# Kernel tuning notes

Measured on AMD Instinct MI355X. Metric: run time of the kernel, lower is better.

The kernel has to match this reference:

```python
import jax, jax.numpy as jnp
import numpy as np

B, H, W, C = 8, 64, 64, 256
NH, WS, SS = 8, 8, 4
HD = C // NH          # head dim 32
N = WS * WS           # 64 tokens per window
NW = (H // WS) * (W // WS)  # 64 windows
MLP = 4 * C


def _rel_index():
    ch = np.arange(WS)
    coords = np.stack(np.meshgrid(ch, ch, indexing='ij')).reshape(2, -1)  # [2, N]
    rel = (coords[:, :, None] - coords[:, None, :]).transpose(1, 2, 0)   # [N, N, 2]
    rel[:, :, 0] += WS - 1
    rel[:, :, 1] += WS - 1
    rel[:, :, 0] *= 2 * WS - 1
    return jnp.asarray(rel.sum(-1))  # [N, N] indices into table

REL_IDX = _rel_index()


def _attn_mask():
    # standard Swin shifted-window mask: [nW, N, N] with 0 / -100
    img = np.zeros((H, W))
    slices = (slice(0, -WS), slice(-WS, -SS), slice(-SS, None))
    cnt = 0
    for hs in slices:
        for ws_ in slices:
            img[hs, ws_] = cnt
            cnt += 1
    m = img.reshape(H // WS, WS, W // WS, WS).transpose(0, 2, 1, 3).reshape(-1, N)
    diff = m[:, None, :] - m[:, :, None]
    return jnp.asarray(np.where(diff != 0, -100.0, 0.0).astype(np.float32))

MASK = _attn_mask()


def setup_inputs() -> dict:
    key = jax.random.key(0)
    ks = jax.random.split(key, 8)
    s = 0.02
    return {
        'hidden_states': jax.random.normal(ks[0], (B, H * W, C), jnp.float32),
        'ln1_g': jnp.ones((C,), jnp.float32),
        'ln1_b': jnp.zeros((C,), jnp.float32),
        'wq': jax.random.normal(ks[1], (C, C), jnp.float32) * s,
        'bq': jnp.zeros((C,), jnp.float32),
        'wk': jax.random.normal(ks[2], (C, C), jnp.float32) * s,
        'bk': jnp.zeros((C,), jnp.float32),
        'wv': jax.random.normal(ks[3], (C, C), jnp.float32) * s,
        'bv': jnp.zeros((C,), jnp.float32),
        'rel_table': jax.random.normal(ks[4], ((2 * WS - 1) ** 2, NH), jnp.float32) * s,
        'wo': jax.random.normal(ks[5], (C, C), jnp.float32) * s,
        'bo': jnp.zeros((C,), jnp.float32),
        'ln2_g': jnp.ones((C,), jnp.float32),
        'ln2_b': jnp.zeros((C,), jnp.float32),
        'w1': jax.random.normal(ks[6], (MLP, C), jnp.float32) * s,
        'b1': jnp.zeros((MLP,), jnp.float32),
        'w2': jax.random.normal(ks[7], (C, MLP), jnp.float32) * s,
        'b2': jnp.zeros((C,), jnp.float32),
    }


def _ln(x, g, b):
    mu = x.mean(-1, keepdims=True)
    var = x.var(-1, keepdims=True)
    return (x - mu) * jax.lax.rsqrt(var + 1e-5) * g + b


def reference(hidden_states, ln1_g, ln1_b, wq, bq, wk, bk, wv, bv, rel_table,
              wo, bo, ln2_g, ln2_b, w1, b1, w2, b2):
    shortcut = hidden_states
    x = _ln(hidden_states, ln1_g, ln1_b).reshape(B, H, W, C)
    # cyclic shift
    x = jnp.roll(x, (-SS, -SS), axis=(1, 2))
    # window partition -> [B*nW, N, C]
    xw = x.reshape(B, H // WS, WS, W // WS, WS, C).transpose(0, 1, 3, 2, 4, 5).reshape(-1, N, C)
    q = (xw @ wq.T + bq).reshape(-1, N, NH, HD).transpose(0, 2, 1, 3)
    k = (xw @ wk.T + bk).reshape(-1, N, NH, HD).transpose(0, 2, 1, 3)
    v = (xw @ wv.T + bv).reshape(-1, N, NH, HD).transpose(0, 2, 1, 3)
    scores = jnp.einsum('bhnd,bhmd->bhnm', q, k) / np.float32(np.sqrt(HD))
    bias = rel_table[REL_IDX]                 # [N, N, NH] gathered bias
    scores = scores + bias.transpose(2, 0, 1)[None]
    scores = scores.reshape(B, NW, NH, N, N) + MASK[None, :, None]
    probs = jax.nn.softmax(scores, axis=-1).reshape(-1, NH, N, N)
    ctx = jnp.einsum('bhnm,bhmd->bnhd', probs, v).reshape(-1, N, C)
    attn_out = ctx @ wo.T + bo                # SelfOutput dense
    # window reverse + reverse shift
    x = attn_out.reshape(B, H // WS, W // WS, WS, WS, C).transpose(0, 1, 3, 2, 4, 5).reshape(B, H, W, C)
    x = jnp.roll(x, (SS, SS), axis=(1, 2)).reshape(B, H * W, C)
    hidden = shortcut + x
    y = _ln(hidden, ln2_g, ln2_b)
    y = jax.nn.gelu(y @ w1.T + b1, approximate=False) @ w2.T + b2
    return hidden + y
```

## Files before the change

kernel.cpp:

```cpp
#include <hip/hip_runtime.h>
#include <hip/hip_bf16.h>
#include <math.h>

__device__ __forceinline__ unsigned short f2bf(float f) {
    union { float f; unsigned u; } c; c.f = f;
    unsigned r = c.u + 0x7fffu + ((c.u >> 16) & 1u);
    return (unsigned short)(r >> 16);
}
__device__ __forceinline__ float bfu(unsigned short u) {
    union { unsigned x; float f; } c; c.x = ((unsigned)u) << 16; return c.f;
}
__device__ __forceinline__ float gelu_t(float x) {
    float z = x * (1.59576912f + 0.07135481f * x * x);
    return x / (1.0f + __expf(-z));
}

typedef __bf16 bf16x8_t __attribute__((ext_vector_type(8)));
typedef float  f32x4_t  __attribute__((ext_vector_type(4)));

#define AS1 __attribute__((address_space(1)))
#define AS3 __attribute__((address_space(3)))
__device__ __forceinline__ void g2lds16(const void* g, void* l) {
    __builtin_amdgcn_global_load_lds((const AS1 unsigned int*)g, (AS3 unsigned int*)l, 16, 0, 0);
}

__global__ void cvt_all(const float* __restrict__ wq, const float* __restrict__ wk,
                        const float* __restrict__ wv, const float* __restrict__ wo,
                        const float* __restrict__ w1, const float* __restrict__ w2,
                        unsigned short* __restrict__ wqkv_b, unsigned short* __restrict__ wo_b,
                        unsigned short* __restrict__ w1_b, unsigned short* __restrict__ w2_b) {
    int i = blockIdx.x * 256 + threadIdx.x;
    const float* src; unsigned short* dst; int base;
    if (i < 16384)       { src = wq; dst = wqkv_b;          base = 0; }
    else if (i < 32768)  { src = wk; dst = wqkv_b + 65536;  base = 16384; }
    else if (i < 49152)  { src = wv; dst = wqkv_b + 131072; base = 32768; }
    else if (i < 65536)  { src = wo; dst = wo_b;            base = 49152; }
    else if (i < 131072) { src = w1; dst = w1_b;            base = 65536; }
    else                 { src = w2; dst = w2_b;            base = 131072; }
    int j = (i - base) * 4;
    float4 v = *(const float4*)(src + j);
    ushort4 o = { f2bf(v.x), f2bf(v.y), f2bf(v.z), f2bf(v.w) };
    *(ushort4*)(dst + j) = o;
}

template<int GATHER, int BF16IN>
__global__ void ln_kernel(const void* __restrict__ xv, const float* __restrict__ g,
                          const float* __restrict__ b, unsigned short* __restrict__ out) {
    int row  = blockIdx.x * 4 + (threadIdx.x >> 6);
    int lane = threadIdx.x & 63;
    int src;
    if (GATHER) {
        int bb = row >> 12;
        int rem = row & 4095;
        int winid = rem >> 6, tok = rem & 63;
        int wi = winid >> 3, wj = winid & 7;
        int ii = tok >> 3,  jj = tok & 7;
        int hh = (wi * 8 + ii + 4) & 63;
        int ww = (wj * 8 + jj + 4) & 63;
        src = (bb << 12) + hh * 64 + ww;
    } else {
        src = row;
    }
    float4 v;
    if (BF16IN) {
        ushort4 u = *(const ushort4*)((const unsigned short*)xv + (size_t)src * 256 + lane * 4);
        v.x = bfu(u.x); v.y = bfu(u.y); v.z = bfu(u.z); v.w = bfu(u.w);
    } else {
        v = *(const float4*)((const float*)xv + (size_t)src * 256 + lane * 4);
    }
    float s  = v.x + v.y + v.z + v.w;
    float s2 = v.x*v.x + v.y*v.y + v.z*v.z + v.w*v.w;
    #pragma unroll
    for (int off = 32; off > 0; off >>= 1) {
        s  += __shfl_xor(s,  off, 64);
        s2 += __shfl_xor(s2, off, 64);
    }
    float mean = s * (1.0f / 256.0f);
    float var  = s2 * (1.0f / 256.0f) - mean * mean;
    float rstd = rsqrtf(var + 1e-5f);
    int c0 = lane * 4;
    float4 gg  = *(const float4*)(g + c0);
    float4 bb4 = *(const float4*)(b + c0);
    ushort4 o;
    o.x = f2bf((v.x - mean) * rstd * gg.x + bb4.x);
    o.y = f2bf((v.y - mean) * rstd * gg.y + bb4.y);
    o.z = f2bf((v.z - mean) * rstd * gg.z + bb4.z);
    o.w = f2bf((v.w - mean) * rstd * gg.w + bb4.w);
    *(ushort4*)(out + (size_t)row * 256 + c0) = o;
}

template<int MODE, int K>
__global__ __launch_bounds__(256, 4) void gemm_tile(
        const unsigned short* __restrict__ A,
        const unsigned short* __restrict__ Bw,
        const float* __restrict__ bias,
        int M, int N,
        unsigned short* __restrict__ obf,
        float* __restrict__ of32,
        const void* __restrict__ addp) {
    __shared__ unsigned short As[128 * 64];
    __shared__ unsigned short Bs[128 * 64];
    const int t = threadIdx.x;
    const int lane = t & 63, wave = t >> 6;
    const int m0 = blockIdx.x * 128, n0 = blockIdx.y * 128;
    const int wm = (wave >> 1) * 64, wn = (wave & 1) * 64;
    const int lr = lane & 15, kg = lane >> 4;

    f32x4_t acc[4][4];
    #pragma unroll
    for (int i = 0; i < 4; ++i)
        #pragma unroll
        for (int j = 0; j < 4; ++j) { acc[i][j][0]=0.f; acc[i][j][1]=0.f; acc[i][j][2]=0.f; acc[i][j][3]=0.f; }

    const int srow = t >> 3;
    const int sc   = (((t & 7) ^ (srow & 7)) * 8);
    const unsigned short* ga = A  + (size_t)(m0 + srow) * K + sc;
    const unsigned short* gb = Bw + (size_t)(n0 + srow) * K + sc;
    unsigned short* la = &As[t * 8];
    unsigned short* lb = &Bs[t * 8];

    #pragma unroll
    for (int k0 = 0; k0 < K; k0 += 64) {
        __syncthreads();
        #pragma unroll
        for (int i = 0; i < 4; ++i) {
            g2lds16(ga + (size_t)(i * 32) * K + k0, la + i * 2048);
            g2lds16(gb + (size_t)(i * 32) * K + k0, lb + i * 2048);
        }
        __syncthreads();
        #pragma unroll
        for (int ks = 0; ks < 64; ks += 32) {
            bf16x8_t af[4], bfr[4];
            #pragma unroll
            for (int i = 0; i < 4; ++i) {
                int r = wm + i * 16 + lr;
                af[i] = *(const bf16x8_t*)&As[r * 64 + ((((ks >> 3) + kg) ^ (r & 7)) << 3)];
            }
            #pragma unroll
            for (int j = 0; j < 4; ++j) {
                int r = wn + j * 16 + lr;
                bfr[j] = *(const bf16x8_t*)&Bs[r * 64 + ((((ks >> 3) + kg) ^ (r & 7)) << 3)];
            }
            #pragma unroll
            for (int i = 0; i < 4; ++i)
                #pragma unroll
                for (int j = 0; j < 4; ++j)
                    acc[i][j] = __builtin_amdgcn_mfma_f32_16x16x32_bf16(af[i], bfr[j], acc[i][j], 0, 0, 0);
        }
    }

    #pragma unroll
    for (int i = 0; i < 4; ++i) {
        #pragma unroll
        for (int j = 0; j < 4; ++j) {
            int col = n0 + wn + j * 16 + lr;
            float bv = bias[col];
            #pragma unroll
            for (int e = 0; e < 4; ++e) {
                int row = m0 + wm + i * 16 + kg * 4 + e;
                float v = acc[i][j][e] + bv;
                if (MODE == 0) {
                    obf[(size_t)row * N + col] = f2bf(v);
                } else if (MODE == 1) {
                    obf[(size_t)row * N + col] = f2bf(gelu_t(v));
                } else if (MODE == 2) {
                    int bb = row >> 12;
                    int rem = row & 4095;
                    int winid = rem >> 6, tok = rem & 63;
                    int wi = winid >> 3, wj = winid & 7;
                    int ii = tok >> 3,  jj = tok & 7;
                    int hh = (wi * 8 + ii + 4) & 63;
                    int ww = (wj * 8 + jj + 4) & 63;
                    size_t dst = ((size_t)(bb << 12) + hh * 64 + ww) * 256 + col;
                    obf[dst] = f2bf(((const float*)addp)[dst] + v);
                } else {
                    size_t dst = (size_t)row * N + col;
                    of32[dst] = bfu(((const unsigned short*)addp)[dst]) + v;
                }
            }
        }
    }
}

#define PR 72
#define VR 72
__global__ void __launch_bounds__(256) attn_mfma(
        const unsigned short* __restrict__ qkv,
        const float* __restrict__ relt,
        unsigned short* __restrict__ ctx) {
    __shared__ float rs[1800];
    __shared__ unsigned short Pl[4][64 * PR];
    __shared__ unsigned short Vt[4][32 * VR];

    int t = threadIdx.x;
    int lane = t & 63, wave = t >> 6;
    for (int i = t; i < 1800; i += 256) rs[i] = relt[i];
    __syncthreads();

    int wh = blockIdx.x * 4 + wave;
    int wg = wh >> 3, h = wh & 7;
    int win = wg & 63;
    int ln = lane & 15, quad = lane >> 4;

    unsigned short* P = &Pl[wave][0];
    unsigned short* V = &Vt[wave][0];
    const unsigned short* base = qkv + (size_t)wg * 64 * 768 + h * 32;

    union BF8 { bf16x8_t v; unsigned short s[8]; };
    {
        const bf16x8_t* vp = (const bf16x8_t*)(base + (size_t)lane * 768 + 512);
        BF8 vv[4];
        #pragma unroll
        for (int c = 0; c < 4; ++c) vv[c].v = vp[c];
        #pragma unroll
        for (int c = 0; c < 4; ++c)
            #pragma unroll
            for (int e = 0; e < 8; ++e)
                V[(c * 8 + e) * VR + lane] = vv[c].s[e];
    }

    bf16x8_t qa[4], kb[4];
    #pragma unroll
    for (int i = 0; i < 4; ++i)
        qa[i] = *(const bf16x8_t*)(base + (size_t)(i * 16 + ln) * 768 + quad * 8);
    #pragma unroll
    for (int j = 0; j < 4; ++j)
        kb[j] = *(const bf16x8_t*)(base + (size_t)(j * 16 + ln) * 768 + 256 + quad * 8);

    f32x4_t acc[4][4];
    #pragma unroll
    for (int i = 0; i < 4; ++i)
        #pragma unroll
        for (int j = 0; j < 4; ++j) { acc[i][j][0]=0.f; acc[i][j][1]=0.f; acc[i][j][2]=0.f; acc[i][j][3]=0.f; }
    #pragma unroll
    for (int i = 0; i < 4; ++i)
        #pragma unroll
        for (int j = 0; j < 4; ++j)
            acc[i][j] = __builtin_amdgcn_mfma_f32_16x16x32_bf16(qa[i], kb[j], acc[i][j], 0, 0, 0);

    const float scale = 0.17677669529663687f;
    int wi = win >> 3, wj = win & 7;
    int mjv = ln & 7;
    int regm[4], mi[4];
    #pragma unroll
    for (int j = 0; j < 4; ++j) {
        mi[j] = j * 2 + (ln >> 3);
        int hm = wi * 8 + mi[j], wm = wj * 8 + mjv;
        regm[j] = (hm < 56 ? 0 : (hm < 60 ? 1 : 2)) * 3 + (wm < 56 ? 0 : (wm < 60 ? 1 : 2));
    }
    float inv[4][4];
    #pragma unroll
    for (int i = 0; i < 4; ++i) {
        #pragma unroll
        for (int e = 0; e < 4; ++e) {
            int q = i * 16 + quad * 4 + e;
            int ti = q >> 3, tj = q & 7;
            int hn = wi * 8 + ti, wn = wj * 8 + tj;
            int regn = (hn < 56 ? 0 : (hn < 60 ? 1 : 2)) * 3 + (wn < 56 ? 0 : (wn < 60 ? 1 : 2));
            float sum = 0.f;
            #pragma unroll
            for (int j = 0; j < 4; ++j) {
                float bv = rs[((ti - mi[j] + 7) * 15 + (tj - mjv + 7)) * 8 + h];
                float s = acc[i][j][e] * scale + bv + (regm[j] != regn ? -100.f : 0.f);
                float p = __expf(s);
                sum += p;
                P[q * PR + j * 16 + ln] = f2bf(p);
            }
            #pragma unroll
            for (int off = 1; off < 16; off <<= 1) sum += __shfl_xor(sum, off, 64);
            inv[i][e] = 1.0f / sum;
        }
    }
    __syncthreads();

    bf16x8_t vb[2][2];
    #pragma unroll
    for (int jd = 0; jd < 2; ++jd)
        #pragma unroll
        for (int kc = 0; kc < 2; ++kc)
            vb[jd][kc] = *(const bf16x8_t*)&V[(jd * 16 + ln) * VR + kc * 32 + quad * 8];
    f32x4_t occ[4][2];
    #pragma unroll
    for (int i = 0; i < 4; ++i)
        #pragma unroll
        for (int jd = 0; jd < 2; ++jd) { occ[i][jd][0]=0.f; occ[i][jd][1]=0.f; occ[i][jd][2]=0.f; occ[i][jd][3]=0.f; }
    #pragma unroll
    for (int i = 0; i < 4; ++i) {
        #pragma unroll
        for (int kc = 0; kc < 2; ++kc) {
            bf16x8_t pf = *(const bf16x8_t*)&P[(i * 16 + ln) * PR + kc * 32 + quad * 8];
            occ[i][0] = __builtin_amdgcn_mfma_f32_16x16x32_bf16(pf, vb[0][kc], occ[i][0], 0, 0, 0);
            occ[i][1] = __builtin_amdgcn_mfma_f32_16x16x32_bf16(pf, vb[1][kc], occ[i][1], 0, 0, 0);
        }
    }

    unsigned short* cbase = ctx + (size_t)wg * 64 * 256 + h * 32;
    #pragma unroll
    for (int i = 0; i < 4; ++i)
        #pragma unroll
        for (int e = 0; e < 4; ++e) {
            int q = i * 16 + quad * 4 + e;
            #pragma unroll
            for (int jd = 0; jd < 2; ++jd)
                cbase[(size_t)q * 256 + jd * 16 + ln] = f2bf(occ[i][jd][e] * inv[i][e]);
        }
}

extern "C" void kernel_launch(void* const* d_in, const int* in_sizes, int n_in,
                              void* d_out, int out_size, void* d_ws, size_t ws_size,
                              hipStream_t stream) {
    const float* hs   = (const float*)d_in[0];
    const float* ln1g = (const float*)d_in[1];
    const float* ln1b = (const float*)d_in[2];
    const float* wq   = (const float*)d_in[3];
    const float* bq   = (const float*)d_in[4];
    const float* wk   = (const float*)d_in[5];
    const float* bk   = (const float*)d_in[6];
    const float* wv   = (const float*)d_in[7];
    const float* bv   = (const float*)d_in[8];
    const float* relt = (const float*)d_in[9];
    const float* wo   = (const float*)d_in[10];
    const float* bo   = (const float*)d_in[11];
    const float* ln2g = (const float*)d_in[12];
    const float* ln2b = (const float*)d_in[13];
    const float* w1   = (const float*)d_in[14];
    const float* b1   = (const float*)d_in[15];
    const float* w2   = (const float*)d_in[16];
    const float* b2   = (const float*)d_in[17];
    float* out = (float*)d_out;

    const size_t NTOK = 32768;
    size_t off = 0;
    auto carve = [&](size_t bytes) { void* p = (char*)d_ws + off; off += (bytes + 255) & ~(size_t)255; return p; };
    unsigned short* wqkv_b = (unsigned short*)carve(768ull * 256 * 2);
    unsigned short* wo_b   = (unsigned short*)carve(65536ull * 2);
    unsigned short* w1_b   = (unsigned short*)carve(262144ull * 2);
    unsigned short* w2_b   = (unsigned short*)carve(262144ull * 2);
    float*          bqkv   = (float*)carve(768ull * 4);
    unsigned short* hiddenb= (unsigned short*)carve(NTOK * 256 * 2);
    unsigned short* xw     = (unsigned short*)carve(NTOK * 256 * 2);
    unsigned short* qkvb   = (unsigned short*)carve(NTOK * 768 * 2);
    unsigned short* cx     = (unsigned short*)carve(NTOK * 256 * 2);
    unsigned short* h1 = qkvb;
    unsigned short* yb = xw;

    cvt_all<<<768, 256, 0, stream>>>(wq, wk, wv, wo, w1, w2, wqkv_b, wo_b, w1_b, w2_b);
    hipMemcpyAsync(bqkv,       bq, 256 * 4, hipMemcpyDeviceToDevice, stream);
    hipMemcpyAsync(bqkv + 256, bk, 256 * 4, hipMemcpyDeviceToDevice, stream);
    hipMemcpyAsync(bqkv + 512, bv, 256 * 4, hipMemcpyDeviceToDevice, stream);

    ln_kernel<1, 0><<<8192, 256, 0, stream>>>(hs, ln1g, ln1b, xw);

    gemm_tile<0, 256><<<dim3(256, 6), 256, 0, stream>>>(xw, wqkv_b, bqkv, 32768, 768, qkvb, nullptr, nullptr);

    attn_mfma<<<1024, 256, 0, stream>>>(qkvb, relt, cx);

    gemm_tile<2, 256><<<dim3(256, 2), 256, 0, stream>>>(cx, wo_b, bo, 32768, 256, hiddenb, nullptr, hs);

    ln_kernel<0, 1><<<8192, 256, 0, stream>>>(hiddenb, ln2g, ln2b, yb);

    gemm_tile<1, 256><<<dim3(256, 8), 256, 0, stream>>>(yb, w1_b, b1, 32768, 1024, h1, nullptr, nullptr);

    gemm_tile<3, 1024><<<dim3(256, 2), 256, 0, stream>>>(h1, w2_b, b2, 32768, 256, nullptr, out, hiddenb);
}
```

Measured before the change: 290.9 us.

## Fuse LN2, MLP up-projection with GELU, and down-projection into one kernel

Replaces the LN2 kernel and the two MLP GEMMs with a single fused kernel. Each block normalises a 64-row tile in LDS, computes the 1024-wide hidden layer in 128-column chunks into LDS, and accumulates the down-projection in registers, so the 32768x1024 intermediate never goes to global memory. Weight fragments are read straight from global memory without LDS staging, and only 512 blocks launch, which may hurt latency hiding and occupancy. The XOR swizzle in gemm_tile's LDS layout is also removed, which may add bank conflicts in the remaining GEMMs.

Measured after the change: 325.9 us. 1.12x slower.

```diff
diff --git a/kernel.cpp b/kernel.cpp
--- a/kernel.cpp
+++ b/kernel.cpp
@@ -43,8 +43,8 @@
     *(ushort4*)(dst + j) = o;
 }
 
-template<int GATHER, int BF16IN>
-__global__ void ln_kernel(const void* __restrict__ xv, const float* __restrict__ g,
+template<int GATHER>
+__global__ void ln_kernel(const float* __restrict__ x, const float* __restrict__ g,
                           const float* __restrict__ b, unsigned short* __restrict__ out) {
     int row  = blockIdx.x * 4 + (threadIdx.x >> 6);
     int lane = threadIdx.x & 63;
@@ -61,13 +61,7 @@
     } else {
         src = row;
     }
-    float4 v;
-    if (BF16IN) {
-        ushort4 u = *(const ushort4*)((const unsigned short*)xv + (size_t)src * 256 + lane * 4);
-        v.x = bfu(u.x); v.y = bfu(u.y); v.z = bfu(u.z); v.w = bfu(u.w);
-    } else {
-        v = *(const float4*)((const float*)xv + (size_t)src * 256 + lane * 4);
-    }
+    const float4 v = *(const float4*)(x + (size_t)src * 256 + lane * 4);
     float s  = v.x + v.y + v.z + v.w;
     float s2 = v.x*v.x + v.y*v.y + v.z*v.z + v.w*v.w;
     #pragma unroll
@@ -96,7 +90,6 @@
         const float* __restrict__ bias,
         int M, int N,
         unsigned short* __restrict__ obf,
-        float* __restrict__ of32,
         const void* __restrict__ addp) {
     __shared__ unsigned short As[128 * 64];
     __shared__ unsigned short Bs[128 * 64];
@@ -113,9 +106,9 @@
         for (int j = 0; j < 4; ++j) { acc[i][j][0]=0.f; acc[i][j][1]=0.f; acc[i][j][2]=0.f; acc[i][j][3]=0.f; }
 
     const int srow = t >> 3;
-    const int sc   = (((t & 7) ^ (srow & 7)) * 8);
-    const unsigned short* ga = A  + (size_t)(m0 + srow) * K + sc;
-    const unsigned short* gb = Bw + (size_t)(n0 + srow) * K + sc;
+    const int sck  = (t & 7) * 8;
+    const unsigned short* ga = A  + (size_t)(m0 + srow) * K + sck;
+    const unsigned short* gb = Bw + (size_t)(n0 + srow) * K + sck;
     unsigned short* la = &As[t * 8];
     unsigned short* lb = &Bs[t * 8];
 
@@ -132,15 +125,11 @@
         for (int ks = 0; ks < 64; ks += 32) {
             bf16x8_t af[4], bfr[4];
             #pragma unroll
-            for (int i = 0; i < 4; ++i) {
-                int r = wm + i * 16 + lr;
-                af[i] = *(const bf16x8_t*)&As[r * 64 + ((((ks >> 3) + kg) ^ (r & 7)) << 3)];
-            }
-            #pragma unroll
-            for (int j = 0; j < 4; ++j) {
-                int r = wn + j * 16 + lr;
-                bfr[j] = *(const bf16x8_t*)&Bs[r * 64 + ((((ks >> 3) + kg) ^ (r & 7)) << 3)];
-            }
+            for (int i = 0; i < 4; ++i)
+                af[i] = *(const bf16x8_t*)&As[(wm + i * 16 + lr) * 64 + ks + kg * 8];
+            #pragma unroll
+            for (int j = 0; j < 4; ++j)
+                bfr[j] = *(const bf16x8_t*)&Bs[(wn + j * 16 + lr) * 64 + ks + kg * 8];
             #pragma unroll
             for (int i = 0; i < 4; ++i)
                 #pragma unroll
@@ -163,7 +152,7 @@
                     obf[(size_t)row * N + col] = f2bf(v);
                 } else if (MODE == 1) {
                     obf[(size_t)row * N + col] = f2bf(gelu_t(v));
-                } else if (MODE == 2) {
+                } else {
                     int bb = row >> 12;
                     int rem = row & 4095;
                     int winid = rem >> 6, tok = rem & 63;
@@ -173,13 +162,144 @@
                     int ww = (wj * 8 + jj + 4) & 63;
                     size_t dst = ((size_t)(bb << 12) + hh * 64 + ww) * 256 + col;
                     obf[dst] = f2bf(((const float*)addp)[dst] + v);
-                } else {
-                    size_t dst = (size_t)row * N + col;
-                    of32[dst] = bfu(((const unsigned short*)addp)[dst]) + v;
                 }
             }
         }
     }
+}
+
+__global__ __launch_bounds__(256, 3) void mlp_fused(
+        const unsigned short* __restrict__ hid,
+        const float* __restrict__ g2, const float* __restrict__ bb2ln,
+        const unsigned short* __restrict__ w1, const float* __restrict__ b1,
+        const unsigned short* __restrict__ w2, const float* __restrict__ b2,
+        float* __restrict__ out) {
+    __shared__ unsigned short Ys[64 * 256];
+    __shared__ unsigned short Hs[64 * 136];
+    const int t = threadIdx.x;
+    const int lane = t & 63, wave = t >> 6;
+    const int m0 = blockIdx.x * 64;
+    const int lr = lane & 15, kg = lane >> 4;
+    const int wm = (wave >> 1) * 32;
+    const int wn1 = (wave & 1) * 64;
+    const int wo2 = (wave & 1) * 128;
+
+    #pragma unroll
+    for (int c = 0; c < 8; ++c)
+        g2lds16(hid + (size_t)(m0 + c * 8 + (t >> 5)) * 256 + (t & 31) * 8,
+                &Ys[c * 2048 + t * 8]);
+    __syncthreads();
+
+    {
+        int r = t >> 2, q = t & 3;
+        unsigned short* rp = &Ys[r * 256 + q * 64];
+        float s = 0.f, s2 = 0.f;
+        #pragma unroll
+        for (int c8 = 0; c8 < 8; ++c8) {
+            bf16x8_t u = *(const bf16x8_t*)(rp + c8 * 8);
+            #pragma unroll
+            for (int e = 0; e < 8; ++e) {
+                float f = (float)u[e];
+                s += f; s2 += f * f;
+            }
+        }
+        s  += __shfl_xor(s, 1, 64);  s  += __shfl_xor(s, 2, 64);
+        s2 += __shfl_xor(s2, 1, 64); s2 += __shfl_xor(s2, 2, 64);
+        float mean = s * (1.0f / 256.0f);
+        float var  = s2 * (1.0f / 256.0f) - mean * mean;
+        float rstd = rsqrtf(var + 1e-5f);
+        #pragma unroll
+        for (int c8 = 0; c8 < 8; ++c8) {
+            int col = q * 64 + c8 * 8;
+            bf16x8_t u = *(const bf16x8_t*)(rp + c8 * 8);
+            float4 ga = *(const float4*)(g2 + col),     gb4 = *(const float4*)(g2 + col + 4);
+            float4 ba = *(const float4*)(bb2ln + col),  bb4 = *(const float4*)(bb2ln + col + 4);
+            unsigned short o[8];
+            o[0] = f2bf(((float)u[0] - mean) * rstd * ga.x + ba.x);
+            o[1] = f2bf(((float)u[1] - mean) * rstd * ga.y + ba.y);
+            o[2] = f2bf(((float)u[2] - mean) * rstd * ga.z + ba.z);
+            o[3] = f2bf(((float)u[3] - mean) * rstd * ga.w + ba.w);
+            o[4] = f2bf(((float)u[4] - mean) * rstd * gb4.x + bb4.x);
+            o[5] = f2bf(((float)u[5] - mean) * rstd * gb4.y + bb4.y);
+            o[6] = f2bf(((float)u[6] - mean) * rstd * gb4.z + bb4.z);
+            o[7] = f2bf(((float)u[7] - mean) * rstd * gb4.w + bb4.w);
+            *(ushort4*)(rp + c8 * 8)     = *(ushort4*)&o[0];
+            *(ushort4*)(rp + c8 * 8 + 4) = *(ushort4*)&o[4];
+        }
+    }
+    __syncthreads();
+
+    f32x4_t acc2[2][8];
+    #pragma unroll
+    for (int i = 0; i < 2; ++i)
+        #pragma unroll
+        for (int j = 0; j < 8; ++j) { acc2[i][j][0]=0.f; acc2[i][j][1]=0.f; acc2[i][j][2]=0.f; acc2[i][j][3]=0.f; }
+
+    for (int c = 0; c < 8; ++c) {
+        const int n0c = c * 128;
+        f32x4_t acc1[2][4];
+        #pragma unroll
+        for (int i = 0; i < 2; ++i)
+            #pragma unroll
+            for (int j = 0; j < 4; ++j) { acc1[i][j][0]=0.f; acc1[i][j][1]=0.f; acc1[i][j][2]=0.f; acc1[i][j][3]=0.f; }
+        #pragma unroll
+        for (int kc = 0; kc < 8; ++kc) {
+            bf16x8_t af[2], bfr[4];
+            #pragma unroll
+            for (int i = 0; i < 2; ++i)
+                af[i] = *(const bf16x8_t*)&Ys[(wm + i * 16 + lr) * 256 + kc * 32 + kg * 8];
+            #pragma unroll
+            for (int j = 0; j < 4; ++j)
+                bfr[j] = *(const bf16x8_t*)(w1 + (size_t)(n0c + wn1 + j * 16 + lr) * 256 + kc * 32 + kg * 8);
+            #pragma unroll
+            for (int i = 0; i < 2; ++i)
+                #pragma unroll
+                for (int j = 0; j < 4; ++j)
+                    acc1[i][j] = __builtin_amdgcn_mfma_f32_16x16x32_bf16(af[i], bfr[j], acc1[i][j], 0, 0, 0);
+        }
+        #pragma unroll
+        for (int i = 0; i < 2; ++i)
+            #pragma unroll
+            for (int j = 0; j < 4; ++j) {
+                float bv = b1[n0c + wn1 + j * 16 + lr];
+                #pragma unroll
+                for (int e = 0; e < 4; ++e) {
+                    int rl = wm + i * 16 + kg * 4 + e;
+                    Hs[rl * 136 + wn1 + j * 16 + lr] = f2bf(gelu_t(acc1[i][j][e] + bv));
+                }
+            }
+        __syncthreads();
+        #pragma unroll
+        for (int kc = 0; kc < 4; ++kc) {
+            bf16x8_t af2[2], bf2[8];
+            #pragma unroll
+            for (int i = 0; i < 2; ++i)
+                af2[i] = *(const bf16x8_t*)&Hs[(wm + i * 16 + lr) * 136 + kc * 32 + kg * 8];
+            #pragma unroll
+            for (int j = 0; j < 8; ++j)
+                bf2[j] = *(const bf16x8_t*)(w2 + (size_t)(wo2 + j * 16 + lr) * 1024 + n0c + kc * 32 + kg * 8);
+            #pragma unroll
+            for (int i = 0; i < 2; ++i)
+                #pragma unroll
+                for (int j = 0; j < 8; ++j)
+                    acc2[i][j] = __builtin_amdgcn_mfma_f32_16x16x32_bf16(af2[i], bf2[j], acc2[i][j], 0, 0, 0);
+        }
+        __syncthreads();
+    }
+
+    #pragma unroll
+    for (int i = 0; i < 2; ++i)
+        #pragma unroll
+        for (int j = 0; j < 8; ++j) {
+            int col = wo2 + j * 16 + lr;
+            float bv = b2[col];
+            #pragma unroll
+            for (int e = 0; e < 4; ++e) {
+                int row = m0 + wm + i * 16 + kg * 4 + e;
+                size_t dst = (size_t)row * 256 + col;
+                out[dst] = acc2[i][j][e] + bv + bfu(hid[dst]);
+            }
+        }
 }
 
 #define PR 72
@@ -341,25 +461,19 @@
     unsigned short* xw     = (unsigned short*)carve(NTOK * 256 * 2);
     unsigned short* qkvb   = (unsigned short*)carve(NTOK * 768 * 2);
     unsigned short* cx     = (unsigned short*)carve(NTOK * 256 * 2);
-    unsigned short* h1 = qkvb;
-    unsigned short* yb = xw;
 
     cvt_all<<<768, 256, 0, stream>>>(wq, wk, wv, wo, w1, w2, wqkv_b, wo_b, w1_b, w2_b);
     hipMemcpyAsync(bqkv,       bq, 256 * 4, hipMemcpyDeviceToDevice, stream);
     hipMemcpyAsync(bqkv + 256, bk, 256 * 4, hipMemcpyDeviceToDevice, stream);
     hipMemcpyAsync(bqkv + 512, bv, 256 * 4, hipMemcpyDeviceToDevice, stream);
 
-    ln_kernel<1, 0><<<8192, 256, 0, stream>>>(hs, ln1g, ln1b, xw);
-
-    gemm_tile<0, 256><<<dim3(256, 6), 256, 0, stream>>>(xw, wqkv_b, bqkv, 32768, 768, qkvb, nullptr, nullptr);
+    ln_kernel<1><<<8192, 256, 0, stream>>>(hs, ln1g, ln1b, xw);
+
+    gemm_tile<0, 256><<<dim3(256, 6), 256, 0, stream>>>(xw, wqkv_b, bqkv, 32768, 768, qkvb, nullptr);
 
     attn_mfma<<<1024, 256, 0, stream>>>(qkvb, relt, cx);
 
-    gemm_tile<2, 256><<<dim3(256, 2), 256, 0, stream>>>(cx, wo_b, bo, 32768, 256, hiddenb, nullptr, hs);
-
-    ln_kernel<0, 1><<<8192, 256, 0, stream>>>(hiddenb, ln2g, ln2b, yb);
-
-    gemm_tile<1, 256><<<dim3(256, 8), 256, 0, stream>>>(yb, w1_b, b1, 32768, 1024, h1, nullptr, nullptr);
-
-    gemm_tile<3, 1024><<<dim3(256, 2), 256, 0, stream>>>(h1, w2_b, b2, 32768, 256, nullptr, out, hiddenb);
-}
+    gemm_tile<2, 256><<<dim3(256, 2), 256, 0, stream>>>(cx, wo_b, bo, 32768, 256, hiddenb, hs);
+
+    mlp_fused<<<512, 256, 0, stream>>>(hiddenb, ln2g, ln2b, w1_b, b1, w2_b, b2, out);
+}
```
